# Kernel optimization log

Hardware: AMD Instinct MI355X
Metric: run time of the kernel (lower is better)

Reference implementation:

```python
import jax, jax.numpy as jnp
import numpy as np


def setup_inputs() -> dict:
    key = jax.random.key(0)
    ks = jax.random.split(key, 7)
    T, B, E = 1024, 256, 128  # max_t, batch, num_evtypes
    x = jax.random.normal(ks[0], (T, B, 2 * E), dtype=jnp.float32)
    h0 = jax.random.normal(ks[1], (B, E), dtype=jnp.float32)
    c0 = jax.random.normal(ks[2], (B, E), dtype=jnp.float32)
    # PyTorch LSTM default init ~ U(-1/sqrt(H), 1/sqrt(H)); use small-scale normals
    s = 1.0 / np.sqrt(E)
    W_ih = jax.random.normal(ks[3], (4 * E, 2 * E), dtype=jnp.float32) * s
    W_hh = jax.random.normal(ks[4], (4 * E, E), dtype=jnp.float32) * s
    b_ih = jax.random.normal(ks[5], (4 * E,), dtype=jnp.float32) * s
    b_hh = jax.random.normal(ks[6], (4 * E,), dtype=jnp.float32) * s
    return {"x": x, "h0": h0, "c0": c0, "W_ih": W_ih, "W_hh": W_hh,
            "b_ih": b_ih, "b_hh": b_hh}


def _lstm(x, h0, c0, W_ih, W_hh, b_ih, b_hh):
    E = h0.shape[-1]
    # precompute input-to-hidden projection for all timesteps: [T, B, 4E]
    x_proj = jnp.einsum('tbi,gi->tbg', x, W_ih) + (b_ih + b_hh)

    def step(carry, xp_t):
        h, c = carry
        gates = xp_t + h @ W_hh.T  # [B, 4E]
        i, f, g, o = jnp.split(gates, 4, axis=-1)  # PyTorch gate order i,f,g,o
        i = jax.nn.sigmoid(i)
        f = jax.nn.sigmoid(f)
        g = jnp.tanh(g)
        o = jax.nn.sigmoid(o)
        c = f * c + i * g
        h = o * jnp.tanh(c)
        return (h, c), h

    _, hs = jax.lax.scan(step, (h0, c0), x_proj)  # hs: [T, B, E]
    return hs


def reference(x, h0, c0, W_ih, W_hh, b_ih, b_hh):
    hs = _lstm(x, h0, c0, W_ih, W_hh, b_ih, b_hh)
    return jax.nn.softplus(hs)
```

## Files before the change

kernel.cpp:

```cpp
#include <hip/hip_runtime.h>
#include <hip/hip_bf16.h>
#include <math.h>

#define T_STEPS 1024
#define BATCH   256
#define E       128
#define K2E     256
#define G4E     512

__device__ __forceinline__ float sigmoidf_fast(float x) {
    return 1.0f / (1.0f + __expf(-x));
}
__device__ __forceinline__ float tanhf_fast(float x) {
    return 1.0f - 2.0f / (1.0f + __expf(2.0f * x));
}
__device__ __forceinline__ float softplusf(float x) {
    return fmaxf(x, 0.0f) + log1pf(__expf(-fabsf(x)));
}

__global__ __launch_bounds__(256)
void xproj_gemm(const float* __restrict__ x, const float* __restrict__ Wih,
                const float* __restrict__ bih, const float* __restrict__ bhh,
                float* __restrict__ xp_f32, __hip_bfloat16* __restrict__ xp_bf16,
                int use_bf16)
{
    __shared__ float As[32][68];
    __shared__ float Bs[32][68];

    const int n0  = blockIdx.x * 64;
    const int m0  = blockIdx.y * 64;
    const int tid = threadIdx.x;
    const int tx  = tid & 15;
    const int ty  = tid >> 4;
    const int lc  = tid & 7;
    const int lr  = tid >> 3;

    float acc[4][4] = {{0.0f}};

    for (int k0 = 0; k0 < K2E; k0 += 32) {
        #pragma unroll
        for (int rr = 0; rr < 2; ++rr) {
            const int r = lr + rr * 32;
            const float4 av = *reinterpret_cast<const float4*>(
                &x[(size_t)(m0 + r) * K2E + k0 + lc * 4]);
            const float4 bv = *reinterpret_cast<const float4*>(
                &Wih[(size_t)(n0 + r) * K2E + k0 + lc * 4]);
            As[lc * 4 + 0][r] = av.x;
            As[lc * 4 + 1][r] = av.y;
            As[lc * 4 + 2][r] = av.z;
            As[lc * 4 + 3][r] = av.w;
            Bs[lc * 4 + 0][r] = bv.x;
            Bs[lc * 4 + 1][r] = bv.y;
            Bs[lc * 4 + 2][r] = bv.z;
            Bs[lc * 4 + 3][r] = bv.w;
        }
        __syncthreads();

        #pragma unroll
        for (int kk = 0; kk < 32; ++kk) {
            const float4 a4 = *reinterpret_cast<const float4*>(&As[kk][ty * 4]);
            const float4 b4 = *reinterpret_cast<const float4*>(&Bs[kk][tx * 4]);
            const float aa[4] = {a4.x, a4.y, a4.z, a4.w};
            const float bb[4] = {b4.x, b4.y, b4.z, b4.w};
            #pragma unroll
            for (int i = 0; i < 4; ++i)
                #pragma unroll
                for (int j = 0; j < 4; ++j)
                    acc[i][j] = fmaf(aa[i], bb[j], acc[i][j]);
        }
        __syncthreads();
    }

    float bsum[4];
    #pragma unroll
    for (int j = 0; j < 4; ++j)
        bsum[j] = bih[n0 + tx * 4 + j] + bhh[n0 + tx * 4 + j];

    #pragma unroll
    for (int i = 0; i < 4; ++i) {
        const size_t row = (size_t)(m0 + ty * 4 + i);
        float4 v;
        v.x = acc[i][0] + bsum[0];
        v.y = acc[i][1] + bsum[1];
        v.z = acc[i][2] + bsum[2];
        v.w = acc[i][3] + bsum[3];
        if (!use_bf16) {
            *reinterpret_cast<float4*>(&xp_f32[row * G4E + n0 + tx * 4]) = v;
        } else {
            __hip_bfloat16* p = &xp_bf16[row * G4E + n0 + tx * 4];
            p[0] = __float2bfloat16(v.x);
            p[1] = __float2bfloat16(v.y);
            p[2] = __float2bfloat16(v.z);
            p[3] = __float2bfloat16(v.w);
        }
    }
}

template<bool XPBF16>
__global__ __launch_bounds__(512, 2)
void lstm_rec(const void* __restrict__ xp_, const float* __restrict__ h0,
              const float* __restrict__ c0, const float* __restrict__ Whh,
              float* __restrict__ out)
{
    const float*           xpf = reinterpret_cast<const float*>(xp_);
    const __hip_bfloat16*  xpb = reinterpret_cast<const __hip_bfloat16*>(xp_);

    const int b = blockIdx.x;
    const int t = threadIdx.x;

    __shared__ __align__(16) float h_lds[E];
    __shared__ __align__(16) float g_lds[G4E];

    float w[E];
    {
        const float4* wr = reinterpret_cast<const float4*>(Whh + (size_t)t * E);
        #pragma unroll
        for (int i = 0; i < E / 4; ++i) {
            const float4 v = wr[i];
            w[4 * i + 0] = v.x;
            w[4 * i + 1] = v.y;
            w[4 * i + 2] = v.z;
            w[4 * i + 3] = v.w;
        }
    }

    float c = 0.0f;
    if (t < E) {
        h_lds[t] = h0[(size_t)b * E + t];
        c        = c0[(size_t)b * E + t];
    }
    __syncthreads();

    float xpv;
    {
        const size_t i0 = (size_t)b * G4E + t;
        xpv = XPBF16 ? __bfloat162float(xpb[i0]) : xpf[i0];
    }

    for (int step = 0; step < T_STEPS; ++step) {
        float xpn = 0.0f;
        if (step + 1 < T_STEPS) {
            const size_t ni = ((size_t)(step + 1) * BATCH + b) * G4E + t;
            xpn = XPBF16 ? __bfloat162float(xpb[ni]) : xpf[ni];
        }

        float acc = xpv;
        const float4* h4 = reinterpret_cast<const float4*>(h_lds);
        #pragma unroll
        for (int i = 0; i < E / 4; ++i) {
            const float4 hv = h4[i];
            acc = fmaf(hv.x, w[4 * i + 0], acc);
            acc = fmaf(hv.y, w[4 * i + 1], acc);
            acc = fmaf(hv.z, w[4 * i + 2], acc);
            acc = fmaf(hv.w, w[4 * i + 3], acc);
        }

        const float a = (t < 2 * E || t >= 3 * E) ? sigmoidf_fast(acc)
                                                  : tanhf_fast(acc);
        if (t >= E) g_lds[t] = a;
        __syncthreads();

        if (t < E) {
            const float gi = a;
            const float gf = g_lds[1 * E + t];
            const float gg = g_lds[2 * E + t];
            const float go = g_lds[3 * E + t];
            c = fmaf(gf, c, gi * gg);
            const float h = go * tanhf_fast(c);
            h_lds[t] = h;
            out[((size_t)step * BATCH + b) * E + t] = softplusf(h);
        }
        __syncthreads();

        xpv = xpn;
    }
}

extern "C" void kernel_launch(void* const* d_in, const int* in_sizes, int n_in,
                              void* d_out, int out_size, void* d_ws, size_t ws_size,
                              hipStream_t stream)
{
    const float* x   = (const float*)d_in[0];
    const float* h0  = (const float*)d_in[1];
    const float* c0  = (const float*)d_in[2];
    const float* Wih = (const float*)d_in[3];
    const float* Whh = (const float*)d_in[4];
    const float* bih = (const float*)d_in[5];
    const float* bhh = (const float*)d_in[6];
    float*       out = (float*)d_out;

    const size_t xp_elems   = (size_t)T_STEPS * BATCH * G4E;
    const bool   ws_fits_f32 = ws_size >= xp_elems * sizeof(float);

    dim3 g1(G4E / 64, (T_STEPS * BATCH) / 64);
    dim3 b1(256);
    xproj_gemm<<<g1, b1, 0, stream>>>(x, Wih, bih, bhh,
                                      (float*)d_ws, (__hip_bfloat16*)d_ws,
                                      ws_fits_f32 ? 0 : 1);

    dim3 g2(BATCH);
    dim3 b2(G4E);
    if (ws_fits_f32)
        lstm_rec<false><<<g2, b2, 0, stream>>>(d_ws, h0, c0, Whh, out);
    else
        lstm_rec<true><<<g2, b2, 0, stream>>>(d_ws, h0, c0, Whh, out);
}
```

Baseline: 2.297 ms.

## Use split-bf16 MFMA for LSTM recurrence and enlarge projection GEMM tiles

```diff
diff --git a/kernel.cpp b/kernel.cpp
--- a/kernel.cpp
+++ b/kernel.cpp
@@ -8,6 +8,10 @@
 #define K2E     256
 #define G4E     512
 
+typedef float  v2f    __attribute__((ext_vector_type(2)));
+typedef float  f32x4  __attribute__((ext_vector_type(4)));
+typedef __bf16 bf16x8 __attribute__((ext_vector_type(8)));
+
 __device__ __forceinline__ float sigmoidf_fast(float x) {
     return 1.0f / (1.0f + __expf(-x));
 }
@@ -17,29 +21,39 @@
 __device__ __forceinline__ float softplusf(float x) {
     return fmaxf(x, 0.0f) + log1pf(__expf(-fabsf(x)));
 }
-
-__global__ __launch_bounds__(256)
+__device__ __forceinline__ unsigned short f2bf_bits(float f) {
+    __bf16 b = (__bf16)f;
+    return __builtin_bit_cast(unsigned short, b);
+}
+__device__ __forceinline__ float bfbits2f(unsigned short u) {
+    return __builtin_bit_cast(float, ((unsigned)u) << 16);
+}
+
+__global__ __launch_bounds__(256, 3)
 void xproj_gemm(const float* __restrict__ x, const float* __restrict__ Wih,
                 const float* __restrict__ bih, const float* __restrict__ bhh,
-                float* __restrict__ xp_f32, __hip_bfloat16* __restrict__ xp_bf16,
-                int use_bf16)
+                float* __restrict__ xp)
 {
-    __shared__ float As[32][68];
-    __shared__ float Bs[32][68];
-
-    const int n0  = blockIdx.x * 64;
-    const int m0  = blockIdx.y * 64;
+    __shared__ float As[32][132];
+    __shared__ float Bs[32][132];
+
+    const int n0  = blockIdx.x * 128;
+    const int m0  = blockIdx.y * 128;
     const int tid = threadIdx.x;
     const int tx  = tid & 15;
     const int ty  = tid >> 4;
     const int lc  = tid & 7;
     const int lr  = tid >> 3;
 
-    float acc[4][4] = {{0.0f}};
+    v2f acc[8][4];
+    #pragma unroll
+    for (int i = 0; i < 8; ++i)
+        #pragma unroll
+        for (int jj = 0; jj < 4; ++jj) acc[i][jj] = (v2f)0.0f;
 
     for (int k0 = 0; k0 < K2E; k0 += 32) {
         #pragma unroll
-        for (int rr = 0; rr < 2; ++rr) {
+        for (int rr = 0; rr < 4; ++rr) {
             const int r = lr + rr * 32;
             const float4 av = *reinterpret_cast<const float4*>(
                 &x[(size_t)(m0 + r) * K2E + k0 + lc * 4]);
@@ -58,121 +72,167 @@
 
         #pragma unroll
         for (int kk = 0; kk < 32; ++kk) {
-            const float4 a4 = *reinterpret_cast<const float4*>(&As[kk][ty * 4]);
-            const float4 b4 = *reinterpret_cast<const float4*>(&Bs[kk][tx * 4]);
-            const float aa[4] = {a4.x, a4.y, a4.z, a4.w};
-            const float bb[4] = {b4.x, b4.y, b4.z, b4.w};
-            #pragma unroll
-            for (int i = 0; i < 4; ++i)
+            const f32x4 a0 = *reinterpret_cast<const f32x4*>(&As[kk][ty * 4]);
+            const f32x4 a1 = *reinterpret_cast<const f32x4*>(&As[kk][64 + ty * 4]);
+            const f32x4 b0 = *reinterpret_cast<const f32x4*>(&Bs[kk][tx * 4]);
+            const f32x4 b1 = *reinterpret_cast<const f32x4*>(&Bs[kk][64 + tx * 4]);
+            const v2f bb0 = {b0.x, b0.y}, bb1 = {b0.z, b0.w};
+            const v2f bb2 = {b1.x, b1.y}, bb3 = {b1.z, b1.w};
+            #pragma unroll
+            for (int i = 0; i < 8; ++i) {
+                const float a = (i < 4) ? a0[i] : a1[i - 4];
+                const v2f av = {a, a};
+                acc[i][0] = __builtin_elementwise_fma(av, bb0, acc[i][0]);
+                acc[i][1] = __builtin_elementwise_fma(av, bb1, acc[i][1]);
+                acc[i][2] = __builtin_elementwise_fma(av, bb2, acc[i][2]);
+                acc[i][3] = __builtin_elementwise_fma(av, bb3, acc[i][3]);
+            }
+        }
+        __syncthreads();
+    }
+
+    float bsum[8];
+    #pragma unroll
+    for (int jj = 0; jj < 4; ++jj) {
+        bsum[jj]     = bih[n0 + tx * 4 + jj]      + bhh[n0 + tx * 4 + jj];
+        bsum[4 + jj] = bih[n0 + 64 + tx * 4 + jj] + bhh[n0 + 64 + tx * 4 + jj];
+    }
+
+    #pragma unroll
+    for (int i = 0; i < 8; ++i) {
+        const size_t row = (size_t)(m0 + ((i < 4) ? (ty * 4 + i) : (64 + ty * 4 + i - 4)));
+        float4 v0, v1;
+        v0.x = acc[i][0][0] + bsum[0];
+        v0.y = acc[i][0][1] + bsum[1];
+        v0.z = acc[i][1][0] + bsum[2];
+        v0.w = acc[i][1][1] + bsum[3];
+        v1.x = acc[i][2][0] + bsum[4];
+        v1.y = acc[i][2][1] + bsum[5];
+        v1.z = acc[i][3][0] + bsum[6];
+        v1.w = acc[i][3][1] + bsum[7];
+        *reinterpret_cast<float4*>(&xp[row * G4E + n0 + tx * 4])      = v0;
+        *reinterpret_cast<float4*>(&xp[row * G4E + n0 + 64 + tx * 4]) = v1;
+    }
+}
+
+__global__ __launch_bounds__(512, 2)
+void lstm_rec_mfma(const float* __restrict__ xp,
+                   const float* __restrict__ h0, const float* __restrict__ c0,
+                   const float* __restrict__ Whh, float* __restrict__ out)
+{
+    __shared__ __align__(16) unsigned short h_lds[2][2][16][128];
+
+    const int tid  = threadIdx.x;
+    const int bb0  = blockIdx.x * 16;
+    const int wid  = tid >> 6;
+    const int lane = tid & 63;
+    const int col  = lane & 15;
+    const int lgrp = lane >> 4;
+    const int j    = wid * 16 + col;
+
+    bf16x8 Whi[4][4], Wlo[4][4];
+    #pragma unroll
+    for (int q = 0; q < 4; ++q) {
+        const float* wr = &Whh[(size_t)(q * 128 + j) * E];
+        #pragma unroll
+        for (int kk = 0; kk < 4; ++kk) {
+            const float4 w0 = *reinterpret_cast<const float4*>(&wr[kk * 32 + lgrp * 8]);
+            const float4 w1 = *reinterpret_cast<const float4*>(&wr[kk * 32 + lgrp * 8 + 4]);
+            const float wv[8] = {w0.x, w0.y, w0.z, w0.w, w1.x, w1.y, w1.z, w1.w};
+            #pragma unroll
+            for (int e = 0; e < 8; ++e) {
+                const __bf16 hi = (__bf16)wv[e];
+                Whi[q][kk][e] = hi;
+                Wlo[q][kk][e] = (__bf16)(wv[e] - (float)hi);
+            }
+        }
+    }
+
+    float c[4];
+    #pragma unroll
+    for (int r = 0; r < 4; ++r)
+        c[r] = c0[(size_t)(bb0 + lgrp * 4 + r) * E + j];
+
+    #pragma unroll
+    for (int s = 0; s < 4; ++s) {
+        const int id  = tid + s * 512;
+        const int row = id >> 7;
+        const int k   = id & 127;
+        const float hv = h0[(size_t)(bb0 + row) * E + k];
+        const unsigned short hb = f2bf_bits(hv);
+        const unsigned short lb = f2bf_bits(hv - bfbits2f(hb));
+        const int sidx = (k + row * 8) & 127;
+        h_lds[0][0][row][sidx] = hb;
+        h_lds[0][1][row][sidx] = lb;
+    }
+
+    float xpre[4][4];
+    #pragma unroll
+    for (int q = 0; q < 4; ++q)
+        #pragma unroll
+        for (int r = 0; r < 4; ++r)
+            xpre[q][r] = xp[(size_t)(bb0 + lgrp * 4 + r) * G4E + q * 128 + j];
+
+    __syncthreads();
+
+    int cur = 0;
+    for (int step = 0; step < T_STEPS; ++step) {
+        f32x4 acc[4];
+        #pragma unroll
+        for (int q = 0; q < 4; ++q)
+            #pragma unroll
+            for (int r = 0; r < 4; ++r)
+                acc[q][r] = xpre[q][r];
+
+        bf16x8 Ahi[4], Alo[4];
+        const int arow = col;
+        #pragma unroll
+        for (int kk = 0; kk < 4; ++kk) {
+            const int idx = (kk * 32 + lgrp * 8 + arow * 8) & 127;
+            Ahi[kk] = *reinterpret_cast<const bf16x8*>(&h_lds[cur][0][arow][idx]);
+            Alo[kk] = *reinterpret_cast<const bf16x8*>(&h_lds[cur][1][arow][idx]);
+        }
+
+        {
+            const int nstep = (step + 1 < T_STEPS) ? step + 1 : 0;
+            #pragma unroll
+            for (int q = 0; q < 4; ++q)
                 #pragma unroll
-                for (int j = 0; j < 4; ++j)
-                    acc[i][j] = fmaf(aa[i], bb[j], acc[i][j]);
+                for (int r = 0; r < 4; ++r)
+                    xpre[q][r] = xp[((size_t)nstep * BATCH + bb0 + lgrp * 4 + r) * G4E
+                                    + q * 128 + j];
+        }
+
+        #pragma unroll
+        for (int kk = 0; kk < 4; ++kk) {
+            #pragma unroll
+            for (int q = 0; q < 4; ++q) {
+                acc[q] = __builtin_amdgcn_mfma_f32_16x16x32_bf16(Ahi[kk], Whi[q][kk], acc[q], 0, 0, 0);
+                acc[q] = __builtin_amdgcn_mfma_f32_16x16x32_bf16(Ahi[kk], Wlo[q][kk], acc[q], 0, 0, 0);
+                acc[q] = __builtin_amdgcn_mfma_f32_16x16x32_bf16(Alo[kk], Whi[q][kk], acc[q], 0, 0, 0);
+            }
+        }
+
+        const int nxt = cur ^ 1;
+        #pragma unroll
+        for (int r = 0; r < 4; ++r) {
+            const float gi = sigmoidf_fast(acc[0][r]);
+            const float gf = sigmoidf_fast(acc[1][r]);
+            const float gg = tanhf_fast(acc[2][r]);
+            const float go = sigmoidf_fast(acc[3][r]);
+            const float cn = fmaf(gf, c[r], gi * gg);
+            c[r] = cn;
+            const float h = go * tanhf_fast(cn);
+            const int row = lgrp * 4 + r;
+            out[((size_t)step * BATCH + bb0 + row) * E + j] = softplusf(h);
+            const unsigned short hb = f2bf_bits(h);
+            const unsigned short lb = f2bf_bits(h - bfbits2f(hb));
+            const int sidx = (j + row * 8) & 127;
+            h_lds[nxt][0][row][sidx] = hb;
+            h_lds[nxt][1][row][sidx] = lb;
         }
         __syncthreads();
-    }
-
-    float bsum[4];
-    #pragma unroll
-    for (int j = 0; j < 4; ++j)
-        bsum[j] = bih[n0 + tx * 4 + j] + bhh[n0 + tx * 4 + j];
-
-    #pragma unroll
-    for (int i = 0; i < 4; ++i) {
-        const size_t row = (size_t)(m0 + ty * 4 + i);
-        float4 v;
-        v.x = acc[i][0] + bsum[0];
-        v.y = acc[i][1] + bsum[1];
-        v.z = acc[i][2] + bsum[2];
-        v.w = acc[i][3] + bsum[3];
-        if (!use_bf16) {
-            *reinterpret_cast<float4*>(&xp_f32[row * G4E + n0 + tx * 4]) = v;
-        } else {
-            __hip_bfloat16* p = &xp_bf16[row * G4E + n0 + tx * 4];
-            p[0] = __float2bfloat16(v.x);
-            p[1] = __float2bfloat16(v.y);
-            p[2] = __float2bfloat16(v.z);
-            p[3] = __float2bfloat16(v.w);
-        }
-    }
-}
-
-template<bool XPBF16>
-__global__ __launch_bounds__(512, 2)
-void lstm_rec(const void* __restrict__ xp_, const float* __restrict__ h0,
-              const float* __restrict__ c0, const float* __restrict__ Whh,
-              float* __restrict__ out)
-{
-    const float*           xpf = reinterpret_cast<const float*>(xp_);
-    const __hip_bfloat16*  xpb = reinterpret_cast<const __hip_bfloat16*>(xp_);
-
-    const int b = blockIdx.x;
-    const int t = threadIdx.x;
-
-    __shared__ __align__(16) float h_lds[E];
-    __shared__ __align__(16) float g_lds[G4E];
-
-    float w[E];
-    {
-        const float4* wr = reinterpret_cast<const float4*>(Whh + (size_t)t * E);
-        #pragma unroll
-        for (int i = 0; i < E / 4; ++i) {
-            const float4 v = wr[i];
-            w[4 * i + 0] = v.x;
-            w[4 * i + 1] = v.y;
-            w[4 * i + 2] = v.z;
-            w[4 * i + 3] = v.w;
-        }
-    }
-
-    float c = 0.0f;
-    if (t < E) {
-        h_lds[t] = h0[(size_t)b * E + t];
-        c        = c0[(size_t)b * E + t];
-    }
-    __syncthreads();
-
-    float xpv;
-    {
-        const size_t i0 = (size_t)b * G4E + t;
-        xpv = XPBF16 ? __bfloat162float(xpb[i0]) : xpf[i0];
-    }
-
-    for (int step = 0; step < T_STEPS; ++step) {
-        float xpn = 0.0f;
-        if (step + 1 < T_STEPS) {
-            const size_t ni = ((size_t)(step + 1) * BATCH + b) * G4E + t;
-            xpn = XPBF16 ? __bfloat162float(xpb[ni]) : xpf[ni];
-        }
-
-        float acc = xpv;
-        const float4* h4 = reinterpret_cast<const float4*>(h_lds);
-        #pragma unroll
-        for (int i = 0; i < E / 4; ++i) {
-            const float4 hv = h4[i];
-            acc = fmaf(hv.x, w[4 * i + 0], acc);
-            acc = fmaf(hv.y, w[4 * i + 1], acc);
-            acc = fmaf(hv.z, w[4 * i + 2], acc);
-            acc = fmaf(hv.w, w[4 * i + 3], acc);
-        }
-
-        const float a = (t < 2 * E || t >= 3 * E) ? sigmoidf_fast(acc)
-                                                  : tanhf_fast(acc);
-        if (t >= E) g_lds[t] = a;
-        __syncthreads();
-
-        if (t < E) {
-            const float gi = a;
-            const float gf = g_lds[1 * E + t];
-            const float gg = g_lds[2 * E + t];
-            const float go = g_lds[3 * E + t];
-            c = fmaf(gf, c, gi * gg);
-            const float h = go * tanhf_fast(c);
-            h_lds[t] = h;
-            out[((size_t)step * BATCH + b) * E + t] = softplusf(h);
-        }
-        __syncthreads();
-
-        xpv = xpn;
+        cur ^= 1;
     }
 }
 
@@ -187,21 +247,12 @@
     const float* Whh = (const float*)d_in[4];
     const float* bih = (const float*)d_in[5];
     const float* bhh = (const float*)d_in[6];
-    float*       out = (float*)d_out;
-
-    const size_t xp_elems   = (size_t)T_STEPS * BATCH * G4E;
-    const bool   ws_fits_f32 = ws_size >= xp_elems * sizeof(float);
-
-    dim3 g1(G4E / 64, (T_STEPS * BATCH) / 64);
-    dim3 b1(256);
-    xproj_gemm<<<g1, b1, 0, stream>>>(x, Wih, bih, bhh,
-                                      (float*)d_ws, (__hip_bfloat16*)d_ws,
-                                      ws_fits_f32 ? 0 : 1);
-
-    dim3 g2(BATCH);
-    dim3 b2(G4E);
-    if (ws_fits_f32)
-        lstm_rec<false><<<g2, b2, 0, stream>>>(d_ws, h0, c0, Whh, out);
-    else
-        lstm_rec<true><<<g2, b2, 0, stream>>>(d_ws, h0, c0, Whh, out);
-}
+
+    float* xp = (float*)d_ws;
+
+    dim3 g1(G4E / 128, (T_STEPS * BATCH) / 128);
+    xproj_gemm<<<g1, dim3(256), 0, stream>>>(x, Wih, bih, bhh, xp);
+
+    lstm_rec_mfma<<<dim3(BATCH / 16), dim3(512), 0, stream>>>(
+        xp, h0, c0, Whh, (float*)d_out);
+}
```

Result: slower. 4.744 ms (+106.5%).
